# Performance work log

Hardware: AMD Instinct MI355X
Metric: run time of the kernel (lower is better)

## Reference

```python
import jax, jax.numpy as jnp
import numpy as np

N_NODES = 50000
N_EDGES = 600000
IN_DIM = 128
HID = 128
N_CLASSES = 40
N_GRAPHS = 128


def setup_inputs() -> dict:
    key = jax.random.key(0)
    ks = jax.random.split(key, 12)
    x = jax.random.normal(ks[0], (N_NODES, IN_DIM), dtype=jnp.float32)
    edge_index = jax.random.randint(ks[1], (2, N_EDGES), 0, N_NODES, dtype=jnp.int64)
    batch = jnp.sort(jax.random.randint(ks[2], (N_NODES,), 0, N_GRAPHS, dtype=jnp.int64))
    dims = [IN_DIM, HID, HID, N_CLASSES]
    params = {}
    for l in range(3):
        d_in, d_out = dims[l], dims[l + 1]
        s = 1.0 / np.sqrt(d_in)
        params[f"Wl{l}"] = jax.random.uniform(ks[3 + 3 * l], (d_out, d_in), jnp.float32, -s, s)
        params[f"bl{l}"] = jax.random.uniform(ks[4 + 3 * l], (d_out,), jnp.float32, -s, s)
        params[f"Wr{l}"] = jax.random.uniform(ks[5 + 3 * l], (d_out, d_in), jnp.float32, -s, s)
    return {"x": x, "edge_index": edge_index, "batch": batch, **params}


def _sage_layer(h, src, dst, Wl, bl, Wr):
    # message: relu(x_j) (edge_attr is None -> zero), mean-aggregate at dst
    m = jnp.maximum(h[src], 0.0)                       # [E, d]
    agg = jax.ops.segment_sum(m, dst, num_segments=N_NODES)
    cnt = jax.ops.segment_sum(jnp.ones((m.shape[0],), h.dtype), dst, num_segments=N_NODES)
    agg = agg / jnp.maximum(cnt, 1.0)[:, None]
    # lin_l(agg) + lin_r(x)
    return agg @ Wl.T + bl + h @ Wr.T


def reference(x, edge_index, batch, Wl0, bl0, Wr0, Wl1, bl1, Wr1, Wl2, bl2, Wr2):
    src, dst = edge_index[0], edge_index[1]
    Ws = [(Wl0, bl0, Wr0), (Wl1, bl1, Wr1), (Wl2, bl2, Wr2)]
    h = x
    for l, (Wl, bl, Wr) in enumerate(Ws):
        # dropout is identity in eval mode
        h = _sage_layer(h, src, dst, Wl, bl, Wr)
        if l != len(Ws) - 1:
            h = jnp.maximum(h, 0.0)
    # global mean pool over graphs
    gsum = jax.ops.segment_sum(h, batch, num_segments=N_GRAPHS)
    gcnt = jax.ops.segment_sum(jnp.ones((h.shape[0],), h.dtype), batch, num_segments=N_GRAPHS)
    g = gsum / jnp.maximum(gcnt, 1.0)[:, None]
    return h, g
```

## Files before the change

### kernel.cpp

```cpp
#include <hip/hip_runtime.h>
#include <hip/hip_bf16.h>


#define NODES 50000
#define K_DIM 128
#define N_GRAPHS 128

typedef __attribute__((ext_vector_type(8))) short short8;
typedef __attribute__((ext_vector_type(4))) short short4v;
typedef __attribute__((ext_vector_type(4))) float f32x4;

__device__ inline short f2bf(float f) {
    unsigned u = __builtin_bit_cast(unsigned, f);
    u += 0x7FFFu + ((u >> 16) & 1u);
    return (short)(u >> 16);
}
__device__ inline float bf2f(short h) {
    unsigned u = ((unsigned)(unsigned short)h) << 16;
    return __builtin_bit_cast(float, u);
}
__device__ inline float blo(unsigned u) { return __builtin_bit_cast(float, u << 16); }
__device__ inline float bhi(unsigned u) { return __builtin_bit_cast(float, u & 0xFFFF0000u); }
__device__ inline unsigned hilo_pack(float f) {
    short h = f2bf(f);
    short l = f2bf(f - bf2f(h));
    return ((unsigned)(unsigned short)h) | (((unsigned)(unsigned short)l) << 16);
}

__global__ void init_kernel(const float* __restrict__ w0, const float* __restrict__ w1,
                            const float* __restrict__ w2, const float* __restrict__ w3,
                            const float* __restrict__ w4, const float* __restrict__ w5,
                            short* __restrict__ whi, short* __restrict__ wlo,
                            int* __restrict__ deg, const int* __restrict__ batch,
                            int* __restrict__ gstart,
                            const float* __restrict__ x, short* __restrict__ xb,
                            float* __restrict__ gsum, int N) {
    int idx = blockIdx.x * 256 + threadIdx.x;
    if (idx < N * (K_DIM / 4)) {
        float4 v = reinterpret_cast<const float4*>(x)[idx];
        short4v b;
        b[0] = f2bf(fmaxf(v.x, 0.f));
        b[1] = f2bf(fmaxf(v.y, 0.f));
        b[2] = f2bf(fmaxf(v.z, 0.f));
        b[3] = f2bf(fmaxf(v.w, 0.f));
        *reinterpret_cast<short4v*>(&xb[idx * 4]) = b;
    }
    if (idx < N) deg[idx] = 0;
    if (idx < N_GRAPHS * 40) gsum[idx] = 0.f;
    const int TOT = 4 * 16384 + 96 * 128;
    if (idx < TOT) {
        float v;
        if (idx < 65536) {
            int m = idx >> 14, e = idx & 16383;
            const float* W = (m == 0) ? w0 : (m == 1) ? w1 : (m == 2) ? w2 : w3;
            v = W[e];
        } else {
            int i2 = idx - 65536;
            int row = i2 >> 7, col = i2 & 127;
            if (row < 40)      v = w4[row * 128 + col];
            else if (row < 80) v = w5[(row - 40) * 128 + col];
            else               v = 0.f;
        }
        unsigned p = hilo_pack(v);
        whi[idx] = (short)(p & 0xFFFFu);
        wlo[idx] = (short)(p >> 16);
    }
    if (idx <= N_GRAPHS) {
        int g = idx;
        int lo = 0, hi = N;
        while (lo < hi) {
            int mid = (lo + hi) >> 1;
            if (batch[mid] < g) lo = mid + 1; else hi = mid;
        }
        gstart[g] = lo;
    }
}

__global__ void deg_kernel(const int* __restrict__ dst, int* __restrict__ deg, int E) {
    int e = blockIdx.x * blockDim.x + threadIdx.x;
    if (e < E) atomicAdd(&deg[dst[e]], 1);
}

__global__ void scan_p1(const int* __restrict__ deg, int* __restrict__ bsum, int N) {
    int i = blockIdx.x * 256 + threadIdx.x;
    int v = (i < N) ? deg[i] : 0;
    #pragma unroll
    for (int off = 32; off > 0; off >>= 1) v += __shfl_down(v, off, 64);
    __shared__ int ws[4];
    int lane = threadIdx.x & 63, wv = threadIdx.x >> 6;
    if (lane == 0) ws[wv] = v;
    __syncthreads();
    if (threadIdx.x == 0) bsum[blockIdx.x] = ws[0] + ws[1] + ws[2] + ws[3];
}

__global__ void scan_p23(const int* __restrict__ deg, const int* __restrict__ bsum,
                         int* __restrict__ rowptr, int* __restrict__ fillpos,
                         int N, int NB) {
    const int tid = threadIdx.x, lane = tid & 63, wv = tid >> 6;
    __shared__ int ws[4];
    __shared__ int sboff[256];
    {
        int v = (tid < NB) ? bsum[tid] : 0;
        int incl = v;
        #pragma unroll
        for (int off = 1; off < 64; off <<= 1) {
            int t = __shfl_up(incl, off, 64);
            if (lane >= off) incl += t;
        }
        if (lane == 63) ws[wv] = incl;
        __syncthreads();
        int add = 0;
        for (int k = 0; k < wv; ++k) add += ws[k];
        sboff[tid] = incl + add - v;
        __syncthreads();
    }
    const int boff = sboff[blockIdx.x];
    int i = blockIdx.x * 256 + tid;
    int v = (i < N) ? deg[i] : 0;
    int incl = v;
    #pragma unroll
    for (int off = 1; off < 64; off <<= 1) {
        int t = __shfl_up(incl, off, 64);
        if (lane >= off) incl += t;
    }
    __shared__ int ws2[4];
    if (lane == 63) ws2[wv] = incl;
    __syncthreads();
    int add = 0;
    for (int k = 0; k < wv; ++k) add += ws2[k];
    int excl = boff + incl + add - v;
    if (i < N) { rowptr[i] = excl; fillpos[i] = excl; }
    if (i == N) rowptr[N] = excl;
}

__global__ void fill_kernel(const int* __restrict__ src, const int* __restrict__ dst,
                            int* __restrict__ fillpos, int* __restrict__ csr_src, int E) {
    int e = blockIdx.x * blockDim.x + threadIdx.x;
    if (e < E) {
        int p = atomicAdd(&fillpos[dst[e]], 1);
        csr_src[p] = src[e];
    }
}

__global__ void agg_bf16(const unsigned short* __restrict__ hb,
                         const int* __restrict__ rowptr,
                         const int* __restrict__ csr_src,
                         short* __restrict__ aggb, int N) {
    int w = (blockIdx.x * blockDim.x + threadIdx.x) >> 6;
    if (w >= N) return;
    int lane = threadIdx.x & 63;
    int half = lane >> 5, l32 = lane & 31;
    int s = rowptr[w], e = rowptr[w + 1];
    float4 acc = make_float4(0.f, 0.f, 0.f, 0.f);
    int i = s + half;
    for (; i + 6 < e; i += 8) {
        int s0 = csr_src[i], s1 = csr_src[i + 2], s2 = csr_src[i + 4], s3 = csr_src[i + 6];
        uint2 v0 = reinterpret_cast<const uint2*>(hb + (size_t)s0 * K_DIM)[l32];
        uint2 v1 = reinterpret_cast<const uint2*>(hb + (size_t)s1 * K_DIM)[l32];
        uint2 v2 = reinterpret_cast<const uint2*>(hb + (size_t)s2 * K_DIM)[l32];
        uint2 v3 = reinterpret_cast<const uint2*>(hb + (size_t)s3 * K_DIM)[l32];
        acc.x += (blo(v0.x) + blo(v1.x)) + (blo(v2.x) + blo(v3.x));
        acc.y += (bhi(v0.x) + bhi(v1.x)) + (bhi(v2.x) + bhi(v3.x));
        acc.z += (blo(v0.y) + blo(v1.y)) + (blo(v2.y) + blo(v3.y));
        acc.w += (bhi(v0.y) + bhi(v1.y)) + (bhi(v2.y) + bhi(v3.y));
    }
    for (; i < e; i += 2) {
        int s0 = csr_src[i];
        uint2 v0 = reinterpret_cast<const uint2*>(hb + (size_t)s0 * K_DIM)[l32];
        acc.x += blo(v0.x); acc.y += bhi(v0.x);
        acc.z += blo(v0.y); acc.w += bhi(v0.y);
    }
    acc.x += __shfl_xor(acc.x, 32, 64);
    acc.y += __shfl_xor(acc.y, 32, 64);
    acc.z += __shfl_xor(acc.z, 32, 64);
    acc.w += __shfl_xor(acc.w, 32, 64);
    if (half == 0) {
        float inv = 1.0f / fmaxf((float)(e - s), 1.0f);
        short4v b;
        b[0] = f2bf(acc.x * inv);
        b[1] = f2bf(acc.y * inv);
        b[2] = f2bf(acc.z * inv);
        b[3] = f2bf(acc.w * inv);
        *reinterpret_cast<short4v*>(&aggb[(size_t)w * K_DIM + l32 * 4]) = b;
    }
}

template<bool XF32>
__global__ __launch_bounds__(256) void sage_mfma_t(
        const short* __restrict__ Ab_in,
        const short* __restrict__ Hhi_in, const short* __restrict__ Hlo_in,
        const float* __restrict__ Xf,
        const short* __restrict__ Bhl, const short* __restrict__ Bll,
        const short* __restrict__ Bhr, const short* __restrict__ Blr,
        const float* __restrict__ bl,
        short* __restrict__ outHi, short* __restrict__ outLo, int N) {
    constexpr int BM = 64;
    constexpr int LSTR = 40;
    const int tid = threadIdx.x;
    const int lane = tid & 63;
    const int wave = tid >> 6;
    const int l15 = lane & 15;
    const int quad = lane >> 4;
    const int m0 = blockIdx.x * BM;
    const int srow = tid >> 2, sc8 = tid & 3;

    __shared__ __align__(16) short Ab [BM * LSTR];
    __shared__ __align__(16) short Ahi[BM * LSTR];
    __shared__ __align__(16) short Alo[BM * LSTR];

    f32x4 acc[4][2];
    #pragma unroll
    for (int i = 0; i < 4; ++i)
        #pragma unroll
        for (int j = 0; j < 2; ++j) acc[i][j] = (f32x4){0.f, 0.f, 0.f, 0.f};

    const short8 zero8 = (short8){0, 0, 0, 0, 0, 0, 0, 0};
    const int sm = m0 + srow;

    for (int k0 = 0; k0 < K_DIM; k0 += 32) {
        __syncthreads();
        {
            short8 va = zero8, vh = zero8, vl = zero8;
            if (sm < N) {
                va = *reinterpret_cast<const short8*>(Ab_in + (size_t)sm * K_DIM + k0 + sc8 * 8);
                if constexpr (XF32) {
                    const float* xp = Xf + (size_t)sm * K_DIM + k0 + sc8 * 8;
                    float4 f0 = *reinterpret_cast<const float4*>(xp);
                    float4 f1 = *reinterpret_cast<const float4*>(xp + 4);
                    float fv[8] = {f0.x, f0.y, f0.z, f0.w, f1.x, f1.y, f1.z, f1.w};
                    #pragma unroll
                    for (int j = 0; j < 8; ++j) {
                        unsigned p = hilo_pack(fv[j]);
                        vh[j] = (short)(p & 0xFFFFu);
                        vl[j] = (short)(p >> 16);
                    }
                } else {
                    vh = *reinterpret_cast<const short8*>(Hhi_in + (size_t)sm * K_DIM + k0 + sc8 * 8);
                    vl = *reinterpret_cast<const short8*>(Hlo_in + (size_t)sm * K_DIM + k0 + sc8 * 8);
                }
            }
            *reinterpret_cast<short8*>(&Ab [srow * LSTR + sc8 * 8]) = va;
            *reinterpret_cast<short8*>(&Ahi[srow * LSTR + sc8 * 8]) = vh;
            *reinterpret_cast<short8*>(&Alo[srow * LSTR + sc8 * 8]) = vl;
        }
        short8 bhl_[2], bll_[2], bhr_[2], blr_[2];
        #pragma unroll
        for (int nt = 0; nt < 2; ++nt) {
            int n = wave * 32 + nt * 16 + l15;
            size_t off = (size_t)n * K_DIM + k0 + quad * 8;
            bhl_[nt] = *reinterpret_cast<const short8*>(Bhl + off);
            bll_[nt] = *reinterpret_cast<const short8*>(Bll + off);
            bhr_[nt] = *reinterpret_cast<const short8*>(Bhr + off);
            blr_[nt] = *reinterpret_cast<const short8*>(Blr + off);
        }
        __syncthreads();
        #pragma unroll
        for (int mt = 0; mt < 4; ++mt) {
            int row = mt * 16 + l15;
            short8 ab = *reinterpret_cast<const short8*>(&Ab [row * LSTR + quad * 8]);
            short8 ah = *reinterpret_cast<const short8*>(&Ahi[row * LSTR + quad * 8]);
            short8 ao = *reinterpret_cast<const short8*>(&Alo[row * LSTR + quad * 8]);
            #pragma unroll
            for (int nt = 0; nt < 2; ++nt) {
                acc[mt][nt] = __builtin_amdgcn_mfma_f32_16x16x32_bf16(ab, bhl_[nt], acc[mt][nt], 0, 0, 0);
                acc[mt][nt] = __builtin_amdgcn_mfma_f32_16x16x32_bf16(ab, bll_[nt], acc[mt][nt], 0, 0, 0);
                acc[mt][nt] = __builtin_amdgcn_mfma_f32_16x16x32_bf16(ah, bhr_[nt], acc[mt][nt], 0, 0, 0);
                acc[mt][nt] = __builtin_amdgcn_mfma_f32_16x16x32_bf16(ah, blr_[nt], acc[mt][nt], 0, 0, 0);
                acc[mt][nt] = __builtin_amdgcn_mfma_f32_16x16x32_bf16(ao, bhr_[nt], acc[mt][nt], 0, 0, 0);
            }
        }
    }

    #pragma unroll
    for (int mt = 0; mt < 4; ++mt) {
        #pragma unroll
        for (int nt = 0; nt < 2; ++nt) {
            int col = wave * 32 + nt * 16 + l15;
            float b = bl[col];
            #pragma unroll
            for (int reg = 0; reg < 4; ++reg) {
                int row = m0 + mt * 16 + quad * 4 + reg;
                if (row < N) {
                    float v = fmaxf(acc[mt][nt][reg] + b, 0.f);
                    unsigned p = hilo_pack(v);
                    outHi[(size_t)row * K_DIM + col] = (short)(p & 0xFFFFu);
                    outLo[(size_t)row * K_DIM + col] = (short)(p >> 16);
                }
            }
        }
    }
}

__global__ __launch_bounds__(256) void gemm80(
        const short* __restrict__ Xhi, const short* __restrict__ Xlo,
        const short* __restrict__ Bh, const short* __restrict__ Bv,
        const float* __restrict__ b2,
        short* __restrict__ ylb, float* __restrict__ yr40, int N) {
    constexpr int BM = 64;
    constexpr int LSTR = 40;
    const int tid = threadIdx.x;
    const int lane = tid & 63;
    const int wave = tid >> 6;
    const int wm = wave & 1;
    const int wn = wave >> 1;
    const int l15 = lane & 15;
    const int quad = lane >> 4;
    const int m0 = blockIdx.x * BM;
    const int srow = tid >> 2, sc8 = tid & 3;

    __shared__ __align__(16) short Ahi[BM * LSTR];
    __shared__ __align__(16) short Alo[BM * LSTR];

    f32x4 acc[2][3];
    #pragma unroll
    for (int i = 0; i < 2; ++i)
        #pragma unroll
        for (int j = 0; j < 3; ++j) acc[i][j] = (f32x4){0.f, 0.f, 0.f, 0.f};

    const short8 zero8 = (short8){0, 0, 0, 0, 0, 0, 0, 0};
    const int sm = m0 + srow;

    for (int k0 = 0; k0 < K_DIM; k0 += 32) {
        __syncthreads();
        {
            short8 vh = zero8, vl = zero8;
            if (sm < N) {
                vh = *reinterpret_cast<const short8*>(Xhi + (size_t)sm * K_DIM + k0 + sc8 * 8);
                vl = *reinterpret_cast<const short8*>(Xlo + (size_t)sm * K_DIM + k0 + sc8 * 8);
            }
            *reinterpret_cast<short8*>(&Ahi[srow * LSTR + sc8 * 8]) = vh;
            *reinterpret_cast<short8*>(&Alo[srow * LSTR + sc8 * 8]) = vl;
        }
        short8 bh[3], bo[3];
        #pragma unroll
        for (int nt = 0; nt < 3; ++nt) {
            int n = wn * 48 + nt * 16 + l15;
            bh[nt] = *reinterpret_cast<const short8*>(Bh + (size_t)n * K_DIM + k0 + quad * 8);
            bo[nt] = *reinterpret_cast<const short8*>(Bv + (size_t)n * K_DIM + k0 + quad * 8);
        }
        __syncthreads();
        #pragma unroll
        for (int mt = 0; mt < 2; ++mt) {
            int row = wm * 32 + mt * 16 + l15;
            short8 ah = *reinterpret_cast<const short8*>(&Ahi[row * LSTR + quad * 8]);
            short8 ao = *reinterpret_cast<const short8*>(&Alo[row * LSTR + quad * 8]);
            #pragma unroll
            for (int nt = 0; nt < 3; ++nt) {
                acc[mt][nt] = __builtin_amdgcn_mfma_f32_16x16x32_bf16(ah, bh[nt], acc[mt][nt], 0, 0, 0);
                acc[mt][nt] = __builtin_amdgcn_mfma_f32_16x16x32_bf16(ah, bo[nt], acc[mt][nt], 0, 0, 0);
                acc[mt][nt] = __builtin_amdgcn_mfma_f32_16x16x32_bf16(ao, bh[nt], acc[mt][nt], 0, 0, 0);
            }
        }
    }

    #pragma unroll
    for (int mt = 0; mt < 2; ++mt) {
        #pragma unroll
        for (int nt = 0; nt < 3; ++nt) {
            int col = wn * 48 + nt * 16 + l15;
            #pragma unroll
            for (int reg = 0; reg < 4; ++reg) {
                int row = m0 + wm * 32 + mt * 16 + quad * 4 + reg;
                if (row < N) {
                    float v = acc[mt][nt][reg];
                    if (col < 40) {
                        ylb[(size_t)row * 40 + col] = f2bf(v);
                    } else if (col < 80) {
                        yr40[(size_t)row * 40 + (col - 40)] = v + b2[col - 40];
                    }
                }
            }
        }
    }
}

__global__ __launch_bounds__(256) void agg40_pool(
        const unsigned int* __restrict__ ylbu, const float* __restrict__ yr40,
        const int* __restrict__ rowptr, const int* __restrict__ csr_src,
        const int* __restrict__ batch, const int* __restrict__ gstart,
        float* __restrict__ out, float* __restrict__ gsum, int N) {
    const int w = (blockIdx.x * blockDim.x + threadIdx.x) >> 6;
    const int lane = threadIdx.x & 63;
    const int wv = threadIdx.x >> 6;
    const int half = lane >> 5, l32 = lane & 31;
    __shared__ float sh[4][40];
    __shared__ int sg[4];
    __shared__ float sinv[4];

    if (w < N) {
        int s = rowptr[w], e = rowptr[w + 1];
        float ax = 0.f, ay = 0.f;
        if (l32 < 20) {
            int i = s + half;
            for (; i + 6 < e; i += 8) {
                int s0 = csr_src[i], s1 = csr_src[i + 2], s2 = csr_src[i + 4], s3 = csr_src[i + 6];
                unsigned v0 = ylbu[(size_t)s0 * 20 + l32];
                unsigned v1 = ylbu[(size_t)s1 * 20 + l32];
                unsigned v2 = ylbu[(size_t)s2 * 20 + l32];
                unsigned v3 = ylbu[(size_t)s3 * 20 + l32];
                ax += (blo(v0) + blo(v1)) + (blo(v2) + blo(v3));
                ay += (bhi(v0) + bhi(v1)) + (bhi(v2) + bhi(v3));
            }
            for (; i < e; i += 2) {
                unsigned v0 = ylbu[(size_t)csr_src[i] * 20 + l32];
                ax += blo(v0); ay += bhi(v0);
            }
        }
        ax += __shfl_xor(ax, 32, 64);
        ay += __shfl_xor(ay, 32, 64);
        if (half == 0 && l32 < 20) {
            float inv = 1.0f / fmaxf((float)(e - s), 1.0f);
            float2 yr = *reinterpret_cast<const float2*>(&yr40[(size_t)w * 40 + 2 * l32]);
            float vx = ax * inv + yr.x;
            float vy = ay * inv + yr.y;
            *reinterpret_cast<float2*>(&out[(size_t)w * 40 + 2 * l32]) = make_float2(vx, vy);
            sh[wv][2 * l32]     = vx;
            sh[wv][2 * l32 + 1] = vy;
        }
    }
    if (lane == 0) {
        if (w < N) {
            int g = batch[w];
            sg[wv] = g;
            sinv[wv] = 1.0f / fmaxf((float)(gstart[g + 1] - gstart[g]), 1.0f);
        } else {
            sg[wv] = -1;
        }
    }
    __syncthreads();
    if (wv == 0 && lane < 40) {
        int cur = -1;
        float accum = 0.f;
        #pragma unroll
        for (int k = 0; k < 4; ++k) {
            int gk = sg[k];
            if (gk < 0) continue;
            float c = sh[k][lane] * sinv[k];
            if (gk == cur) {
                accum += c;
            } else {
                if (cur >= 0) atomicAdd(&gsum[cur * 40 + lane], accum);
                cur = gk;
                accum = c;
            }
        }
        if (cur >= 0) atomicAdd(&gsum[cur * 40 + lane], accum);
    }
}

extern "C" void kernel_launch(void* const* d_in, const int* in_sizes, int n_in,
                              void* d_out, int out_size, void* d_ws, size_t ws_size,
                              hipStream_t stream) {
    const float* x    = (const float*)d_in[0];
    const int*   ei   = (const int*)d_in[1];
    const int*   batch= (const int*)d_in[2];
    const float* Wl0  = (const float*)d_in[3];
    const float* bl0  = (const float*)d_in[4];
    const float* Wr0  = (const float*)d_in[5];
    const float* Wl1  = (const float*)d_in[6];
    const float* bl1  = (const float*)d_in[7];
    const float* Wr1  = (const float*)d_in[8];
    const float* Wl2  = (const float*)d_in[9];
    const float* bl2  = (const float*)d_in[10];
    const float* Wr2  = (const float*)d_in[11];

    const int N = in_sizes[0] / K_DIM;
    const int E = in_sizes[1] / 2;
    const int* src = ei;
    const int* dst = ei + E;

    float* out = (float*)d_out;
    float* gsum = out + (size_t)N * 40;

    char* w = (char*)d_ws;
    auto alloc = [&](size_t bytes) {
        char* p = w;
        w += (bytes + 255) & ~(size_t)255;
        return p;
    };
    const size_t PL = (size_t)N * K_DIM * 2;
    short* aggb  = (short*)alloc(PL);
    short* xb    = (short*)alloc(PL);
    short* h1hi  = (short*)alloc(PL);
    short* h1lo  = (short*)alloc(PL);
    short* h2hi  = (short*)alloc(PL);
    short* h2lo  = (short*)alloc(PL);
    short* ylb   = (short*)alloc((size_t)N * 40 * 2);
    float* yr40  = (float*)alloc((size_t)N * 40 * 4);
    int*   rowptr= (int*)alloc((size_t)(N + 1) * 4);
    int*   deg   = (int*)alloc((size_t)N * 4);
    int*   fillp = (int*)alloc((size_t)N * 4);
    int*   csr   = (int*)alloc((size_t)E * 4);
    int*   bsum  = (int*)alloc(256 * 4);
    int*   gstart= (int*)alloc((size_t)(N_GRAPHS + 1) * 4);
    short* whi   = (short*)alloc(77824 * 2);
    short* wlo   = (short*)alloc(77824 * 2);

    const int NB = (N + 255) / 256;
    const int initGrid = (N * (K_DIM / 4) + 255) / 256;

    init_kernel<<<initGrid, 256, 0, stream>>>(Wl0, Wr0, Wl1, Wr1, Wl2, Wr2,
                                              whi, wlo, deg, batch, gstart,
                                              x, xb, gsum, N);
    deg_kernel<<<(E + 255) / 256, 256, 0, stream>>>(dst, deg, E);
    scan_p1<<<NB, 256, 0, stream>>>(deg, bsum, N);
    scan_p23<<<NB, 256, 0, stream>>>(deg, bsum, rowptr, fillp, N, NB);
    fill_kernel<<<(E + 255) / 256, 256, 0, stream>>>(src, dst, fillp, csr, E);

    short* hWl0 = whi;          short* lWl0 = wlo;
    short* hWr0 = whi + 16384;  short* lWr0 = wlo + 16384;
    short* hWl1 = whi + 32768;  short* lWl1 = wlo + 32768;
    short* hWr1 = whi + 49152;  short* lWr1 = wlo + 49152;
    short* hW2  = whi + 65536;  short* lW2  = wlo + 65536;

    const int aggGrid  = (N * 64 + 255) / 256;
    const int gemmGrid = (N + 63) / 64;

    agg_bf16<<<aggGrid, 256, 0, stream>>>((const unsigned short*)xb, rowptr, csr, aggb, N);
    sage_mfma_t<true><<<gemmGrid, 256, 0, stream>>>(
        aggb, nullptr, nullptr, x, hWl0, lWl0, hWr0, lWr0, bl0, h1hi, h1lo, N);
    agg_bf16<<<aggGrid, 256, 0, stream>>>((const unsigned short*)h1hi, rowptr, csr, aggb, N);
    sage_mfma_t<false><<<gemmGrid, 256, 0, stream>>>(
        aggb, h1hi, h1lo, nullptr, hWl1, lWl1, hWr1, lWr1, bl1, h2hi, h2lo, N);
    gemm80<<<gemmGrid, 256, 0, stream>>>(h2hi, h2lo, hW2, lW2, bl2, ylb, yr40, N);
    agg40_pool<<<aggGrid, 256, 0, stream>>>((const unsigned int*)ylb, yr40,
                                            rowptr, csr, batch, gstart, out, gsum, N);
}
```

Before: 326.8 us.

## Replace two-pass scan with atomic block offsets and widen aggregation loads to 16B

Replaces the two-kernel prefix scan with a single kernel where each block claims its segment base through an atomicAdd on a global counter. Nodes' CSR segments are then unordered across blocks, so row ends come from rowptr+deg instead of rowptr[w+1]. The bf16 aggregation kernel is also changed to use four edge slots per wave with 16-byte loads per lane instead of two slots with 8-byte loads, which gives more gathers in flight. Segment placement in memory now varies between runs, so summation order within a node's neighbors may also vary.

```diff
diff --git a/kernel.cpp b/kernel.cpp
--- a/kernel.cpp
+++ b/kernel.cpp
@@ -32,7 +32,7 @@
                             const float* __restrict__ w4, const float* __restrict__ w5,
                             short* __restrict__ whi, short* __restrict__ wlo,
                             int* __restrict__ deg, const int* __restrict__ batch,
-                            int* __restrict__ gstart,
+                            int* __restrict__ gstart, int* __restrict__ counter,
                             const float* __restrict__ x, short* __restrict__ xb,
                             float* __restrict__ gsum, int N) {
     int idx = blockIdx.x * 256 + threadIdx.x;
@@ -47,6 +47,7 @@
     }
     if (idx < N) deg[idx] = 0;
     if (idx < N_GRAPHS * 40) gsum[idx] = 0.f;
+    if (idx == 0) *counter = 0;
     const int TOT = 4 * 16384 + 96 * 128;
     if (idx < TOT) {
         float v;
@@ -81,40 +82,9 @@
     if (e < E) atomicAdd(&deg[dst[e]], 1);
 }
 
-__global__ void scan_p1(const int* __restrict__ deg, int* __restrict__ bsum, int N) {
-    int i = blockIdx.x * 256 + threadIdx.x;
-    int v = (i < N) ? deg[i] : 0;
-    #pragma unroll
-    for (int off = 32; off > 0; off >>= 1) v += __shfl_down(v, off, 64);
-    __shared__ int ws[4];
-    int lane = threadIdx.x & 63, wv = threadIdx.x >> 6;
-    if (lane == 0) ws[wv] = v;
-    __syncthreads();
-    if (threadIdx.x == 0) bsum[blockIdx.x] = ws[0] + ws[1] + ws[2] + ws[3];
-}
-
-__global__ void scan_p23(const int* __restrict__ deg, const int* __restrict__ bsum,
-                         int* __restrict__ rowptr, int* __restrict__ fillpos,
-                         int N, int NB) {
+__global__ void csr_offsets(const int* __restrict__ deg, int* __restrict__ counter,
+                            int* __restrict__ rowptr, int* __restrict__ fillpos, int N) {
     const int tid = threadIdx.x, lane = tid & 63, wv = tid >> 6;
-    __shared__ int ws[4];
-    __shared__ int sboff[256];
-    {
-        int v = (tid < NB) ? bsum[tid] : 0;
-        int incl = v;
-        #pragma unroll
-        for (int off = 1; off < 64; off <<= 1) {
-            int t = __shfl_up(incl, off, 64);
-            if (lane >= off) incl += t;
-        }
-        if (lane == 63) ws[wv] = incl;
-        __syncthreads();
-        int add = 0;
-        for (int k = 0; k < wv; ++k) add += ws[k];
-        sboff[tid] = incl + add - v;
-        __syncthreads();
-    }
-    const int boff = sboff[blockIdx.x];
     int i = blockIdx.x * 256 + tid;
     int v = (i < N) ? deg[i] : 0;
     int incl = v;
@@ -123,14 +93,16 @@
         int t = __shfl_up(incl, off, 64);
         if (lane >= off) incl += t;
     }
-    __shared__ int ws2[4];
-    if (lane == 63) ws2[wv] = incl;
+    __shared__ int ws[4];
+    __shared__ int sbase;
+    if (lane == 63) ws[wv] = incl;
     __syncthreads();
-    int add = 0;
-    for (int k = 0; k < wv; ++k) add += ws2[k];
-    int excl = boff + incl + add - v;
+    if (tid == 0) sbase = atomicAdd(counter, ws[0] + ws[1] + ws[2] + ws[3]);
+    __syncthreads();
+    int add = sbase;
+    for (int k = 0; k < wv; ++k) add += ws[k];
+    int excl = add + incl - v;
     if (i < N) { rowptr[i] = excl; fillpos[i] = excl; }
-    if (i == N) rowptr[N] = excl;
 }
 
 __global__ void fill_kernel(const int* __restrict__ src, const int* __restrict__ dst,
@@ -143,45 +115,48 @@
 }
 
 __global__ void agg_bf16(const unsigned short* __restrict__ hb,
-                         const int* __restrict__ rowptr,
+                         const int* __restrict__ rowptr, const int* __restrict__ deg,
                          const int* __restrict__ csr_src,
                          short* __restrict__ aggb, int N) {
     int w = (blockIdx.x * blockDim.x + threadIdx.x) >> 6;
     if (w >= N) return;
     int lane = threadIdx.x & 63;
-    int half = lane >> 5, l32 = lane & 31;
-    int s = rowptr[w], e = rowptr[w + 1];
-    float4 acc = make_float4(0.f, 0.f, 0.f, 0.f);
-    int i = s + half;
-    for (; i + 6 < e; i += 8) {
-        int s0 = csr_src[i], s1 = csr_src[i + 2], s2 = csr_src[i + 4], s3 = csr_src[i + 6];
-        uint2 v0 = reinterpret_cast<const uint2*>(hb + (size_t)s0 * K_DIM)[l32];
-        uint2 v1 = reinterpret_cast<const uint2*>(hb + (size_t)s1 * K_DIM)[l32];
-        uint2 v2 = reinterpret_cast<const uint2*>(hb + (size_t)s2 * K_DIM)[l32];
-        uint2 v3 = reinterpret_cast<const uint2*>(hb + (size_t)s3 * K_DIM)[l32];
-        acc.x += (blo(v0.x) + blo(v1.x)) + (blo(v2.x) + blo(v3.x));
-        acc.y += (bhi(v0.x) + bhi(v1.x)) + (bhi(v2.x) + bhi(v3.x));
-        acc.z += (blo(v0.y) + blo(v1.y)) + (blo(v2.y) + blo(v3.y));
-        acc.w += (bhi(v0.y) + bhi(v1.y)) + (bhi(v2.y) + bhi(v3.y));
-    }
-    for (; i < e; i += 2) {
-        int s0 = csr_src[i];
-        uint2 v0 = reinterpret_cast<const uint2*>(hb + (size_t)s0 * K_DIM)[l32];
-        acc.x += blo(v0.x); acc.y += bhi(v0.x);
-        acc.z += blo(v0.y); acc.w += bhi(v0.y);
-    }
-    acc.x += __shfl_xor(acc.x, 32, 64);
-    acc.y += __shfl_xor(acc.y, 32, 64);
-    acc.z += __shfl_xor(acc.z, 32, 64);
-    acc.w += __shfl_xor(acc.w, 32, 64);
-    if (half == 0) {
+    int slot = lane >> 4, l16 = lane & 15;
+    int s = rowptr[w];
+    int e = s + deg[w];
+    const uint4* T = reinterpret_cast<const uint4*>(hb);
+    float2 a0 = make_float2(0.f, 0.f), a1 = a0, a2 = a0, a3 = a0;
+    int i = s + slot;
+    for (; i + 4 < e; i += 8) {
+        uint4 va = T[(size_t)csr_src[i] * 16 + l16];
+        uint4 vb = T[(size_t)csr_src[i + 4] * 16 + l16];
+        a0.x += blo(va.x) + blo(vb.x); a0.y += bhi(va.x) + bhi(vb.x);
+        a1.x += blo(va.y) + blo(vb.y); a1.y += bhi(va.y) + bhi(vb.y);
+        a2.x += blo(va.z) + blo(vb.z); a2.y += bhi(va.z) + bhi(vb.z);
+        a3.x += blo(va.w) + blo(vb.w); a3.y += bhi(va.w) + bhi(vb.w);
+    }
+    for (; i < e; i += 4) {
+        uint4 va = T[(size_t)csr_src[i] * 16 + l16];
+        a0.x += blo(va.x); a0.y += bhi(va.x);
+        a1.x += blo(va.y); a1.y += bhi(va.y);
+        a2.x += blo(va.z); a2.y += bhi(va.z);
+        a3.x += blo(va.w); a3.y += bhi(va.w);
+    }
+    #pragma unroll
+    for (int off = 16; off <= 32; off <<= 1) {
+        a0.x += __shfl_xor(a0.x, off, 64); a0.y += __shfl_xor(a0.y, off, 64);
+        a1.x += __shfl_xor(a1.x, off, 64); a1.y += __shfl_xor(a1.y, off, 64);
+        a2.x += __shfl_xor(a2.x, off, 64); a2.y += __shfl_xor(a2.y, off, 64);
+        a3.x += __shfl_xor(a3.x, off, 64); a3.y += __shfl_xor(a3.y, off, 64);
+    }
+    if (slot == 0) {
         float inv = 1.0f / fmaxf((float)(e - s), 1.0f);
-        short4v b;
-        b[0] = f2bf(acc.x * inv);
-        b[1] = f2bf(acc.y * inv);
-        b[2] = f2bf(acc.z * inv);
-        b[3] = f2bf(acc.w * inv);
-        *reinterpret_cast<short4v*>(&aggb[(size_t)w * K_DIM + l32 * 4]) = b;
+        short8 b;
+        b[0] = f2bf(a0.x * inv); b[1] = f2bf(a0.y * inv);
+        b[2] = f2bf(a1.x * inv); b[3] = f2bf(a1.y * inv);
+        b[4] = f2bf(a2.x * inv); b[5] = f2bf(a2.y * inv);
+        b[6] = f2bf(a3.x * inv); b[7] = f2bf(a3.y * inv);
+        *reinterpret_cast<short8*>(&aggb[(size_t)w * K_DIM + l16 * 8]) = b;
     }
 }
 
@@ -376,7 +351,8 @@
 
 __global__ __launch_bounds__(256) void agg40_pool(
         const unsigned int* __restrict__ ylbu, const float* __restrict__ yr40,
-        const int* __restrict__ rowptr, const int* __restrict__ csr_src,
+        const int* __restrict__ rowptr, const int* __restrict__ deg,
+        const int* __restrict__ csr_src,
         const int* __restrict__ batch, const int* __restrict__ gstart,
         float* __restrict__ out, float* __restrict__ gsum, int N) {
     const int w = (blockIdx.x * blockDim.x + threadIdx.x) >> 6;
@@ -388,7 +364,7 @@
     __shared__ float sinv[4];
 
     if (w < N) {
-        int s = rowptr[w], e = rowptr[w + 1];
+        int s = rowptr[w], e = s + deg[w];
         float ax = 0.f, ay = 0.f;
         if (l32 < 20) {
             int i = s + half;
@@ -491,7 +467,7 @@
     int*   deg   = (int*)alloc((size_t)N * 4);
     int*   fillp = (int*)alloc((size_t)N * 4);
     int*   csr   = (int*)alloc((size_t)E * 4);
-    int*   bsum  = (int*)alloc(256 * 4);
+    int*   counter = (int*)alloc(256);
     int*   gstart= (int*)alloc((size_t)(N_GRAPHS + 1) * 4);
     short* whi   = (short*)alloc(77824 * 2);
     short* wlo   = (short*)alloc(77824 * 2);
@@ -500,11 +476,10 @@
     const int initGrid = (N * (K_DIM / 4) + 255) / 256;
 
     init_kernel<<<initGrid, 256, 0, stream>>>(Wl0, Wr0, Wl1, Wr1, Wl2, Wr2,
-                                              whi, wlo, deg, batch, gstart,
+                                              whi, wlo, deg, batch, gstart, counter,
                                               x, xb, gsum, N);
     deg_kernel<<<(E + 255) / 256, 256, 0, stream>>>(dst, deg, E);
-    scan_p1<<<NB, 256, 0, stream>>>(deg, bsum, N);
-    scan_p23<<<NB, 256, 0, stream>>>(deg, bsum, rowptr, fillp, N, NB);
+    csr_offsets<<<NB, 256, 0, stream>>>(deg, counter, rowptr, fillp, N);
     fill_kernel<<<(E + 255) / 256, 256, 0, stream>>>(src, dst, fillp, csr, E);
 
     short* hWl0 = whi;          short* lWl0 = wlo;
@@ -516,13 +491,13 @@
     const int aggGrid  = (N * 64 + 255) / 256;
     const int gemmGrid = (N + 63) / 64;
 
-    agg_bf16<<<aggGrid, 256, 0, stream>>>((const unsigned short*)xb, rowptr, csr, aggb, N);
+    agg_bf16<<<aggGrid, 256, 0, stream>>>((const unsigned short*)xb, rowptr, deg, csr, aggb, N);
     sage_mfma_t<true><<<gemmGrid, 256, 0, stream>>>(
         aggb, nullptr, nullptr, x, hWl0, lWl0, hWr0, lWr0, bl0, h1hi, h1lo, N);
-    agg_bf16<<<aggGrid, 256, 0, stream>>>((const unsigned short*)h1hi, rowptr, csr, aggb, N);
+    agg_bf16<<<aggGrid, 256, 0, stream>>>((const unsigned short*)h1hi, rowptr, deg, csr, aggb, N);
     sage_mfma_t<false><<<gemmGrid, 256, 0, stream>>>(
         aggb, h1hi, h1lo, nullptr, hWl1, lWl1, hWr1, lWr1, bl1, h2hi, h2lo, N);
     gemm80<<<gemmGrid, 256, 0, stream>>>(h2hi, h2lo, hW2, lW2, bl2, ylb, yr40, N);
     agg40_pool<<<aggGrid, 256, 0, stream>>>((const unsigned int*)ylb, yr40,
-                                            rowptr, csr, batch, gstart, out, gsum, N);
-}
+                                            rowptr, deg, csr, batch, gstart, out, gsum, N);
+}
```

Measured after the change: 325.0 us. Within noise of the previous version (-0.6%).
